# Kernel tuning notes

Measured on AMD Instinct MI355X. Metric: run time of the kernel, lower is better.

The kernel has to match this reference:

```python
import jax, jax.numpy as jnp
import numpy as np

E = 200000      # number of edge tokens
M = 3200000     # number of e2e attention pairs
IN_DIM = 64
EMBED = 64
H = 8
D = EMBED // H


def setup_inputs() -> dict:
    key = jax.random.key(0)
    ks = jax.random.split(key, 12)
    s = 1.0 / np.sqrt(IN_DIM)
    inp = {
        "edge_features": jax.random.normal(ks[0], (E, IN_DIM), dtype=jnp.float32),
        "e2e": jax.random.randint(ks[1], (2, M), 0, E, dtype=jnp.int32),
        "attn_bias": jax.random.normal(ks[2], (M, H), dtype=jnp.float32),
        "Wq": jax.random.uniform(ks[3], (IN_DIM, EMBED), jnp.float32, -s, s),
        "bq": jax.random.uniform(ks[4], (EMBED,), jnp.float32, -s, s),
        "Wk": jax.random.uniform(ks[5], (IN_DIM, EMBED), jnp.float32, -s, s),
        "bk": jax.random.uniform(ks[6], (EMBED,), jnp.float32, -s, s),
        "Wv": jax.random.uniform(ks[7], (IN_DIM, EMBED), jnp.float32, -s, s),
        "bv": jax.random.uniform(ks[8], (EMBED,), jnp.float32, -s, s),
        "Wo": jax.random.uniform(ks[9], (EMBED, EMBED), jnp.float32, -s, s),
        "bo": jax.random.uniform(ks[10], (EMBED,), jnp.float32, -s, s),
    }
    return inp


def _segment_softmax(logits, index, num_segments):
    # logits: (M, H) grouped by index (dst edge id)
    seg_max = jax.ops.segment_max(logits, index, num_segments=num_segments)
    seg_max = jnp.where(jnp.isfinite(seg_max), seg_max, 0.0)  # empty segments
    ex = jnp.exp(logits - seg_max[index])
    seg_sum = jax.ops.segment_sum(ex, index, num_segments=num_segments)
    return ex / (seg_sum[index] + 1e-16)


def reference(edge_features, e2e, attn_bias, Wq, bq, Wk, bk, Wv, bv, Wo, bo):
    src_e, dst_e = e2e[0], e2e[1]
    scale = D ** (-0.5)
    q = (edge_features @ Wq + bq).reshape(E, H, D)
    k = (edge_features @ Wk + bk).reshape(E, H, D)
    v = (edge_features @ Wv + bv).reshape(E, H, D)
    q_dst = q[dst_e]                       # (M, H, D) gather
    k_src = k[src_e]                       # (M, H, D) gather
    logits = jnp.sum(q_dst * k_src, axis=-1) * scale   # (M, H)
    logits = logits + attn_bias
    attn = _segment_softmax(logits, dst_e, E)          # (M, H)
    msg = v[src_e] * attn[..., None]                   # (M, H, D)
    out = jax.ops.segment_sum(msg, dst_e, num_segments=E)  # (E, H, D)
    out = out.reshape(E, EMBED)
    return out @ Wo + bo
```

## Files before the change

kernel.cpp:

```cpp
#include <hip/hip_runtime.h>

#define E_N 200000
#define M_N 3200000
#define SCAN_CHUNK 2048
#define NB1 98

#define NBUCK 782
#define NCHUNK 1000
#define CH 3200
#define BLEN (NBUCK * NCHUNK)
#define NB2 382
#define NP 4
#define SMAX 8192

typedef __attribute__((ext_vector_type(8))) short bf16x8;
typedef __attribute__((ext_vector_type(4))) float f32x4;
typedef __attribute__((ext_vector_type(8))) _Float16 f16x8;

__device__ __forceinline__ short f2bf(float f) {
    union { float f; unsigned u; } x; x.f = f;
    unsigned r = x.u + 0x7fffu + ((x.u >> 16) & 1u);
    return (short)(r >> 16);
}

__global__ __launch_bounds__(256) void qkv_mfma(
    const float* __restrict__ x,
    const float* __restrict__ Wq, const float* __restrict__ bq,
    const float* __restrict__ Wk, const float* __restrict__ bk,
    const float* __restrict__ Wv, const float* __restrict__ bv,
    float* __restrict__ q, _Float16* __restrict__ k, _Float16* __restrict__ v)
{
    const int w    = threadIdx.x >> 6;
    const int lane = threadIdx.x & 63;
    const int quad = lane >> 4;
    const int m    = lane & 15;

    bf16x8 Bq[4][2], Bk[4][2], Bv[4][2];
    float  bqv[4], bkv[4], bvv[4];
    #pragma unroll
    for (int ct = 0; ct < 4; ct++) {
        int cc = ct * 16 + m;
        bqv[ct] = bq[cc]; bkv[ct] = bk[cc]; bvv[ct] = bv[cc];
        #pragma unroll
        for (int kb = 0; kb < 2; kb++) {
            #pragma unroll
            for (int j = 0; j < 8; j++) {
                int kk = kb * 32 + quad * 8 + j;
                Bq[ct][kb][j] = f2bf(Wq[kk * 64 + cc]);
                Bk[ct][kb][j] = f2bf(Wk[kk * 64 + cc]);
                Bv[ct][kb][j] = f2bf(Wv[kk * 64 + cc]);
            }
        }
    }

    for (int row0 = blockIdx.x * 64 + w * 16; row0 < E_N; row0 += gridDim.x * 64) {
        const float* xr = x + (long long)(row0 + m) * 64 + quad * 8;
        bf16x8 A[2];
        #pragma unroll
        for (int kb = 0; kb < 2; kb++) {
            float4 p0 = *(const float4*)(xr + kb * 32);
            float4 p1 = *(const float4*)(xr + kb * 32 + 4);
            A[kb][0] = f2bf(p0.x); A[kb][1] = f2bf(p0.y);
            A[kb][2] = f2bf(p0.z); A[kb][3] = f2bf(p0.w);
            A[kb][4] = f2bf(p1.x); A[kb][5] = f2bf(p1.y);
            A[kb][6] = f2bf(p1.z); A[kb][7] = f2bf(p1.w);
        }

        #pragma unroll
        for (int ct = 0; ct < 4; ct++) {
            f32x4 aq = {bqv[ct], bqv[ct], bqv[ct], bqv[ct]};
            f32x4 ak = {bkv[ct], bkv[ct], bkv[ct], bkv[ct]};
            f32x4 av = {bvv[ct], bvv[ct], bvv[ct], bvv[ct]};
            aq = __builtin_amdgcn_mfma_f32_16x16x32_bf16(A[0], Bq[ct][0], aq, 0, 0, 0);
            aq = __builtin_amdgcn_mfma_f32_16x16x32_bf16(A[1], Bq[ct][1], aq, 0, 0, 0);
            ak = __builtin_amdgcn_mfma_f32_16x16x32_bf16(A[0], Bk[ct][0], ak, 0, 0, 0);
            ak = __builtin_amdgcn_mfma_f32_16x16x32_bf16(A[1], Bk[ct][1], ak, 0, 0, 0);
            av = __builtin_amdgcn_mfma_f32_16x16x32_bf16(A[0], Bv[ct][0], av, 0, 0, 0);
            av = __builtin_amdgcn_mfma_f32_16x16x32_bf16(A[1], Bv[ct][1], av, 0, 0, 0);
            #pragma unroll
            for (int i = 0; i < 4; i++) {
                long long off = (long long)(row0 + quad * 4 + i) * 64 + ct * 16 + m;
                q[off] = aq[i];
                k[off] = (_Float16)ak[i];
                v[off] = (_Float16)av[i];
            }
        }
    }
}

__global__ __launch_bounds__(256) void hist_kernel(
    const int* __restrict__ e2e, int* __restrict__ counts)
{
    int m4 = (blockIdx.x * 256 + threadIdx.x) * 4;
    if (m4 < M_N) {
        int4 d = *(const int4*)(e2e + M_N + m4);
        atomicAdd(&counts[d.x], 1);
        atomicAdd(&counts[d.y], 1);
        atomicAdd(&counts[d.z], 1);
        atomicAdd(&counts[d.w], 1);
    }
}

__global__ __launch_bounds__(256) void scan1_kernel(
    const int* __restrict__ counts, int* __restrict__ cursor,
    int* __restrict__ blocksums, int len)
{
    __shared__ int s[256];
    const int t = threadIdx.x;
    const int base = blockIdx.x * SCAN_CHUNK + t * 8;

    int vals[8];
    int tot = 0;
    #pragma unroll
    for (int j = 0; j < 8; j++) {
        int idx = base + j;
        vals[j] = (idx < len) ? counts[idx] : 0;
        tot += vals[j];
    }
    s[t] = tot;
    __syncthreads();
    for (int off = 1; off < 256; off <<= 1) {
        int add = (t >= off) ? s[t - off] : 0;
        __syncthreads();
        s[t] += add;
        __syncthreads();
    }
    int excl = (t == 0) ? 0 : s[t - 1];
    if (t == 255) blocksums[blockIdx.x] = s[255];

    int run = excl;
    #pragma unroll
    for (int j = 0; j < 8; j++) {
        int idx = base + j;
        if (idx < len) cursor[idx] = run;
        run += vals[j];
    }
}

__global__ __launch_bounds__(256) void scan2_kernel(
    const int* __restrict__ blocksums, int* __restrict__ blockoff, int nb)
{
    __shared__ int s[256];
    const int t = threadIdx.x;
    int vals[4];
    int tot = 0;
    #pragma unroll
    for (int u = 0; u < 4; u++) {
        int idx = t * 4 + u;
        vals[u] = (idx < nb) ? blocksums[idx] : 0;
        tot += vals[u];
    }
    s[t] = tot;
    __syncthreads();
    for (int off = 1; off < 256; off <<= 1) {
        int add = (t >= off) ? s[t - off] : 0;
        __syncthreads();
        s[t] += add;
        __syncthreads();
    }
    int run = (t == 0) ? 0 : s[t - 1];
    #pragma unroll
    for (int u = 0; u < 4; u++) {
        int idx = t * 4 + u;
        if (idx < nb) blockoff[idx] = run;
        run += vals[u];
    }
}

__global__ __launch_bounds__(1024) void bhist_kernel(
    const int* __restrict__ e2e, int* __restrict__ bcnt)
{
    __shared__ int lc[NBUCK];
    const int c = blockIdx.x;
    for (int i = threadIdx.x; i < NBUCK; i += 1024) lc[i] = 0;
    __syncthreads();
    const int m0 = c * CH;
    for (int i = threadIdx.x * 4; i < CH; i += 4096) {
        int4 d = *(const int4*)(e2e + M_N + m0 + i);
        atomicAdd(&lc[d.x >> 8], 1);
        atomicAdd(&lc[d.y >> 8], 1);
        atomicAdd(&lc[d.z >> 8], 1);
        atomicAdd(&lc[d.w >> 8], 1);
    }
    __syncthreads();
    for (int i = threadIdx.x; i < NBUCK; i += 1024) bcnt[i * NCHUNK + c] = lc[i];
}

__global__ __launch_bounds__(1024, 4) void scatter_bucket(
    const int* __restrict__ e2e, const float* __restrict__ bias,
    const int* __restrict__ bcur0, const int* __restrict__ boff2,
    int* __restrict__ meta, _Float16* __restrict__ bias_s)
{
    __shared__ int gbase[NBUCK];
    __shared__ unsigned short bk[CH];
    __shared__ char pool[CH * 16] __attribute__((aligned(16)));
    int*   cnt     = (int*)pool;
    int*   s       = (int*)(pool + 4096);
    f16x8* stage_b = (f16x8*)pool;
    int*   stage_m = (int*)pool;

    const int c = blockIdx.x;
    const int t = threadIdx.x;
    const int m0 = c * CH;

    for (int b = t; b < NBUCK; b += 1024) {
        cnt[b] = 0;
        int idx = b * NCHUNK + c;
        gbase[b] = bcur0[idx] + boff2[idx >> 11];
    }
    __syncthreads();

    int   mt[NP];
    int   pk[NP];
    f16x8 bb[NP];
    #pragma unroll
    for (int r = 0; r < NP; r++) {
        int i = t + r * 1024;
        pk[r] = -1;
        if (i < CH) {
            int m = m0 + i;
            int dst = e2e[M_N + m];
            int src = e2e[m];
            int b = dst >> 8;
            pk[r] = b << 12;
            mt[r] = ((dst & 255) << 18) | src;
            float4 b0 = *(const float4*)(bias + (long long)m * 8);
            float4 b1 = *(const float4*)(bias + (long long)m * 8 + 4);
            f16x8 xx;
            xx[0] = (_Float16)b0.x; xx[1] = (_Float16)b0.y;
            xx[2] = (_Float16)b0.z; xx[3] = (_Float16)b0.w;
            xx[4] = (_Float16)b1.x; xx[5] = (_Float16)b1.y;
            xx[6] = (_Float16)b1.z; xx[7] = (_Float16)b1.w;
            bb[r] = xx;
            atomicAdd(&cnt[b], 1);
        }
    }
    __syncthreads();

    int v = (t < NBUCK) ? cnt[t] : 0;
    s[t] = v;
    __syncthreads();
    for (int off = 1; off < 1024; off <<= 1) {
        int add = (t >= off) ? s[t - off] : 0;
        __syncthreads();
        s[t] += add;
        __syncthreads();
    }
    if (t < NBUCK) {
        int excl = (t == 0) ? 0 : s[t - 1];
        gbase[t] -= excl;
        cnt[t] = excl;
    }
    __syncthreads();

    #pragma unroll
    for (int r = 0; r < NP; r++) {
        if (pk[r] >= 0) {
            int b = pk[r] >> 12;
            int j = atomicAdd(&cnt[b], 1);
            pk[r] = (b << 12) | j;
        }
    }
    __syncthreads();

    #pragma unroll
    for (int r = 0; r < NP; r++) {
        if (pk[r] >= 0) {
            int j = pk[r] & 4095;
            stage_b[j] = bb[r];
            bk[j] = (unsigned short)(pk[r] >> 12);
        }
    }
    __syncthreads();
    for (int j = t; j < CH; j += 1024) {
        int slot = gbase[bk[j]] + j;
        *(f16x8*)(bias_s + (long long)slot * 8) = stage_b[j];
    }
    __syncthreads();

    #pragma unroll
    for (int r = 0; r < NP; r++) {
        if (pk[r] >= 0) stage_m[pk[r] & 4095] = mt[r];
    }
    __syncthreads();
    for (int j = t; j < CH; j += 1024) {
        meta[gbase[bk[j]] + j] = stage_m[j];
    }
}

__global__ __launch_bounds__(512, 2) void bucket_permute(
    const int* __restrict__ cursor, const int* __restrict__ boff,
    int* __restrict__ meta, _Float16* __restrict__ bias_s)
{
    __shared__ int smeta[SMAX];
    __shared__ int cnt[256];
    __shared__ int scn[256];
    const int b = blockIdx.x;
    const int t = threadIdx.x;
    const int d0 = b << 8;
    const int bs = cursor[d0] + boff[d0 >> 11];
    const int d1 = d0 + 256;
    const int be = (d1 < E_N) ? (cursor[d1] + boff[d1 >> 11]) : M_N;
    int n = be - bs;
    if (n > SMAX) n = SMAX;

    if (t < 256) cnt[t] = 0;
    __syncthreads();
    #pragma unroll
    for (int r = 0; r < SMAX / 512; r++) {
        int i = t + r * 512;
        if (i < n) {
            int mm = meta[bs + i];
            smeta[i] = mm;
            atomicAdd(&cnt[mm >> 18], 1);
        }
    }
    __syncthreads();
    if (t < 256) scn[t] = cnt[t];
    __syncthreads();
    for (int off = 1; off < 256; off <<= 1) {
        int v = 0;
        if (t < 256 && t >= off) v = scn[t - off];
        __syncthreads();
        if (t < 256) scn[t] += v;
        __syncthreads();
    }
    if (t < 256) cnt[t] = scn[t] - cnt[t];
    __syncthreads();

    int    pos[SMAX / 512];
    f16x8  bb[SMAX / 512];
    #pragma unroll
    for (int r = 0; r < SMAX / 512; r++) {
        int i = t + r * 512;
        if (i < n) {
            int mm = smeta[i];
            pos[r] = bs + atomicAdd(&cnt[mm >> 18], 1);
            bb[r]  = *(const f16x8*)(bias_s + (long long)(bs + i) * 8);
        }
    }
    __syncthreads();
    #pragma unroll
    for (int r = 0; r < SMAX / 512; r++) {
        int i = t + r * 512;
        if (i < n) {
            meta[pos[r]] = smeta[i] & 0x3FFFF;
            *(f16x8*)(bias_s + (long long)pos[r] * 8) = bb[r];
        }
    }
}

__global__ __launch_bounds__(256) void aggregate_kernel(
    const _Float16* __restrict__ k, const _Float16* __restrict__ v,
    const _Float16* __restrict__ bias_s,
    const int* __restrict__ counts, const int* __restrict__ cursor,
    const int* __restrict__ blockoff,
    const int* __restrict__ sorted,
    float* __restrict__ qmsg)
{
    const int wid  = threadIdx.x >> 6;
    const int lane = threadIdx.x & 63;
    const int ps   = lane >> 3;
    const int t    = lane & 7;

    for (int e = blockIdx.x * 4 + wid; e < E_N; e += gridDim.x * 4) {
        float qv = qmsg[(long long)e * 64 + lane];
        float qs[8];
        #pragma unroll
        for (int j = 0; j < 8; j++) qs[j] = __shfl(qv, t * 8 + j, 64);

        int start = cursor[e] + blockoff[e >> 11];
        int cnt   = counts[e];
        int end   = start + cnt;

        float acc[8] = {0.f,0.f,0.f,0.f,0.f,0.f,0.f,0.f};
        float ws = 0.0f;

        for (int i = start; i < end; i += 16) {
            int iA = i + ps;
            int iB = i + 8 + ps;
            bool vA = iA < end, vB = iB < end;
            int cA = vA ? iA : start;
            int cB = vB ? iB : start;
            int sA = sorted[cA];
            int sB = sorted[cB];
            float bA = (float)bias_s[(long long)cA * 8 + t];
            float bB = (float)bias_s[(long long)cB * 8 + t];
            f16x8 kA = *(const f16x8*)(k + (long long)sA * 64 + t * 8);
            f16x8 kB = *(const f16x8*)(k + (long long)sB * 64 + t * 8);
            f16x8 vA8 = *(const f16x8*)(v + (long long)sA * 64 + t * 8);
            f16x8 vB8 = *(const f16x8*)(v + (long long)sB * 64 + t * 8);

            float dA = 0.0f, dB = 0.0f;
            #pragma unroll
            for (int j = 0; j < 8; j++) {
                dA = fmaf(qs[j], (float)kA[j], dA);
                dB = fmaf(qs[j], (float)kB[j], dB);
            }
            float wA = vA ? __expf(fmaf(dA, 0.35355339059327373f, bA)) : 0.0f;
            float wB = vB ? __expf(fmaf(dB, 0.35355339059327373f, bB)) : 0.0f;
            ws += wA + wB;
            #pragma unroll
            for (int j = 0; j < 8; j++) {
                acc[j] = fmaf(wA, (float)vA8[j], acc[j]);
                acc[j] = fmaf(wB, (float)vB8[j], acc[j]);
            }
        }

        #pragma unroll
        for (int st = 8; st <= 32; st <<= 1) {
            #pragma unroll
            for (int j = 0; j < 8; j++) acc[j] += __shfl_xor(acc[j], st, 64);
            ws += __shfl_xor(ws, st, 64);
        }

        if (ps == 0) {
            float inv = 1.0f / (ws + 1e-16f);
            float4 o0, o1;
            o0.x = acc[0]*inv; o0.y = acc[1]*inv;
            o0.z = acc[2]*inv; o0.w = acc[3]*inv;
            o1.x = acc[4]*inv; o1.y = acc[5]*inv;
            o1.z = acc[6]*inv; o1.w = acc[7]*inv;
            *(float4*)(qmsg + (long long)e * 64 + t * 8)     = o0;
            *(float4*)(qmsg + (long long)e * 64 + t * 8 + 4) = o1;
        }
    }
}

__global__ __launch_bounds__(256) void out_mfma(
    const float* __restrict__ Wo, const float* __restrict__ bo,
    float* __restrict__ out)
{
    const int w    = threadIdx.x >> 6;
    const int lane = threadIdx.x & 63;
    const int quad = lane >> 4;
    const int m    = lane & 15;

    bf16x8 B[4][2];
    float  bov[4];
    #pragma unroll
    for (int ct = 0; ct < 4; ct++) {
        int cc = ct * 16 + m;
        bov[ct] = bo[cc];
        #pragma unroll
        for (int kb = 0; kb < 2; kb++) {
            #pragma unroll
            for (int j = 0; j < 8; j++) {
                int kk = kb * 32 + quad * 8 + j;
                B[ct][kb][j] = f2bf(Wo[kk * 64 + cc]);
            }
        }
    }

    for (int row0 = blockIdx.x * 64 + w * 16; row0 < E_N; row0 += gridDim.x * 64) {
        const float* xr = out + (long long)(row0 + m) * 64 + quad * 8;
        bf16x8 A[2];
        #pragma unroll
        for (int kb = 0; kb < 2; kb++) {
            float4 p0 = *(const float4*)(xr + kb * 32);
            float4 p1 = *(const float4*)(xr + kb * 32 + 4);
            A[kb][0] = f2bf(p0.x); A[kb][1] = f2bf(p0.y);
            A[kb][2] = f2bf(p0.z); A[kb][3] = f2bf(p0.w);
            A[kb][4] = f2bf(p1.x); A[kb][5] = f2bf(p1.y);
            A[kb][6] = f2bf(p1.z); A[kb][7] = f2bf(p1.w);
        }

        f32x4 acc[4];
        #pragma unroll
        for (int ct = 0; ct < 4; ct++) {
            acc[ct] = (f32x4){bov[ct], bov[ct], bov[ct], bov[ct]};
            acc[ct] = __builtin_amdgcn_mfma_f32_16x16x32_bf16(A[0], B[ct][0], acc[ct], 0, 0, 0);
            acc[ct] = __builtin_amdgcn_mfma_f32_16x16x32_bf16(A[1], B[ct][1], acc[ct], 0, 0, 0);
        }
        #pragma unroll
        for (int ct = 0; ct < 4; ct++) {
            #pragma unroll
            for (int i = 0; i < 4; i++) {
                out[(long long)(row0 + quad * 4 + i) * 64 + ct * 16 + m] = acc[ct][i];
            }
        }
    }
}

extern "C" void kernel_launch(void* const* d_in, const int* in_sizes, int n_in,
                              void* d_out, int out_size, void* d_ws, size_t ws_size,
                              hipStream_t stream) {
    const float* x    = (const float*)d_in[0];
    const int*   e2e  = (const int*)  d_in[1];
    const float* bias = (const float*)d_in[2];
    const float* Wq   = (const float*)d_in[3];
    const float* bq   = (const float*)d_in[4];
    const float* Wk   = (const float*)d_in[5];
    const float* bk   = (const float*)d_in[6];
    const float* Wv   = (const float*)d_in[7];
    const float* bv   = (const float*)d_in[8];
    const float* Wo   = (const float*)d_in[9];
    const float* bo   = (const float*)d_in[10];
    float* out = (float*)d_out;

    _Float16* kh     = (_Float16*)d_ws;
    _Float16* vh     = kh + (long long)E_N * 64;
    int*      counts = (int*)(vh + (long long)E_N * 64);
    int*      cursor = counts + E_N;
    int*      bsum   = cursor + E_N;
    int*      boff   = bsum + 512;
    int*      sorted = boff + 512;
    _Float16* bias_s = (_Float16*)(sorted + M_N);
    int*      bcnt   = (int*)(bias_s + (long long)M_N * 8);
    int*      bsum2  = bcnt + BLEN;
    int*      boff2  = bsum2 + 512;

    hipMemsetAsync(counts, 0, (size_t)E_N * sizeof(int), stream);

    qkv_mfma<<<640, 256, 0, stream>>>(x, Wq, bq, Wk, bk, Wv, bv, out, kh, vh);

    hist_kernel<<<M_N / 1024, 256, 0, stream>>>(e2e, counts);
    scan1_kernel<<<NB1, 256, 0, stream>>>(counts, cursor, bsum, E_N);
    scan2_kernel<<<1, 256, 0, stream>>>(bsum, boff, NB1);

    bhist_kernel<<<NCHUNK, 1024, 0, stream>>>(e2e, bcnt);
    scan1_kernel<<<NB2, 256, 0, stream>>>(bcnt, bcnt, bsum2, BLEN);
    scan2_kernel<<<1, 256, 0, stream>>>(bsum2, boff2, NB2);

    scatter_bucket<<<NCHUNK, 1024, 0, stream>>>(e2e, bias, bcnt, boff2,
                                                sorted, bias_s);
    bucket_permute<<<NBUCK, 512, 0, stream>>>(cursor, boff, sorted, bias_s);

    aggregate_kernel<<<8192, 256, 0, stream>>>(kh, vh, bias_s, counts, cursor,
                                               boff, sorted, out);

    out_mfma<<<640, 256, 0, stream>>>(Wo, bo, out);
}
```

Before: 652.1 us.

## Fuse bucket permute into aggregation and drop global per-edge histogram/scan

Removes the global per-destination histogram, scan and the bucket_permute pass. Each 256-destination bucket block now counting-sorts its entries in shared memory into a local order array and aggregates directly from it. Bucket bounds come from the existing bucket histogram scan. This cuts several kernel launches and a full global rewrite of the sorted meta/bias arrays. The cost is far fewer blocks (782 of 512 threads) doing aggregation, so occupancy and load balance are lower, and bias is now read with an indirect, uncoalesced access pattern.

```diff
diff --git a/kernel.cpp b/kernel.cpp
--- a/kernel.cpp
+++ b/kernel.cpp
@@ -3,7 +3,6 @@
 #define E_N 200000
 #define M_N 3200000
 #define SCAN_CHUNK 2048
-#define NB1 98
 
 #define NBUCK 782
 #define NCHUNK 1000
@@ -85,19 +84,6 @@
                 v[off] = (_Float16)av[i];
             }
         }
-    }
-}
-
-__global__ __launch_bounds__(256) void hist_kernel(
-    const int* __restrict__ e2e, int* __restrict__ counts)
-{
-    int m4 = (blockIdx.x * 256 + threadIdx.x) * 4;
-    if (m4 < M_N) {
-        int4 d = *(const int4*)(e2e + M_N + m4);
-        atomicAdd(&counts[d.x], 1);
-        atomicAdd(&counts[d.y], 1);
-        atomicAdd(&counts[d.z], 1);
-        atomicAdd(&counts[d.w], 1);
     }
 }
 
@@ -288,19 +274,30 @@
     }
 }
 
-__global__ __launch_bounds__(512, 2) void bucket_permute(
-    const int* __restrict__ cursor, const int* __restrict__ boff,
-    int* __restrict__ meta, _Float16* __restrict__ bias_s)
+__global__ __launch_bounds__(512, 2) void aggregate_bucket(
+    const _Float16* __restrict__ k, const _Float16* __restrict__ v,
+    const _Float16* __restrict__ bias_s,
+    const int* __restrict__ bstart, const int* __restrict__ boff2,
+    const int* __restrict__ meta,
+    float* __restrict__ qmsg)
 {
     __shared__ int smeta[SMAX];
+    __shared__ unsigned short ord[SMAX];
     __shared__ int cnt[256];
     __shared__ int scn[256];
+    __shared__ int base[256];
     const int b = blockIdx.x;
     const int t = threadIdx.x;
-    const int d0 = b << 8;
-    const int bs = cursor[d0] + boff[d0 >> 11];
-    const int d1 = d0 + 256;
-    const int be = (d1 < E_N) ? (cursor[d1] + boff[d1 >> 11]) : M_N;
+
+    const int i0 = b * NCHUNK;
+    const int bs = bstart[i0] + boff2[i0 >> 11];
+    int be;
+    if (b + 1 < NBUCK) {
+        int i1 = (b + 1) * NCHUNK;
+        be = bstart[i1] + boff2[i1 >> 11];
+    } else {
+        be = M_N;
+    }
     int n = be - bs;
     if (n > SMAX) n = SMAX;
 
@@ -319,77 +316,66 @@
     if (t < 256) scn[t] = cnt[t];
     __syncthreads();
     for (int off = 1; off < 256; off <<= 1) {
-        int v = 0;
-        if (t < 256 && t >= off) v = scn[t - off];
-        __syncthreads();
-        if (t < 256) scn[t] += v;
-        __syncthreads();
-    }
-    if (t < 256) cnt[t] = scn[t] - cnt[t];
-    __syncthreads();
-
-    int    pos[SMAX / 512];
-    f16x8  bb[SMAX / 512];
+        int vv = 0;
+        if (t < 256 && t >= off) vv = scn[t - off];
+        __syncthreads();
+        if (t < 256) scn[t] += vv;
+        __syncthreads();
+    }
+    if (t < 256) {
+        int excl = scn[t] - cnt[t];
+        base[t] = excl;
+        cnt[t]  = excl;
+    }
+    __syncthreads();
     #pragma unroll
     for (int r = 0; r < SMAX / 512; r++) {
         int i = t + r * 512;
         if (i < n) {
-            int mm = smeta[i];
-            pos[r] = bs + atomicAdd(&cnt[mm >> 18], 1);
-            bb[r]  = *(const f16x8*)(bias_s + (long long)(bs + i) * 8);
-        }
-    }
-    __syncthreads();
-    #pragma unroll
-    for (int r = 0; r < SMAX / 512; r++) {
-        int i = t + r * 512;
-        if (i < n) {
-            meta[pos[r]] = smeta[i] & 0x3FFFF;
-            *(f16x8*)(bias_s + (long long)pos[r] * 8) = bb[r];
-        }
-    }
-}
-
-__global__ __launch_bounds__(256) void aggregate_kernel(
-    const _Float16* __restrict__ k, const _Float16* __restrict__ v,
-    const _Float16* __restrict__ bias_s,
-    const int* __restrict__ counts, const int* __restrict__ cursor,
-    const int* __restrict__ blockoff,
-    const int* __restrict__ sorted,
-    float* __restrict__ qmsg)
-{
-    const int wid  = threadIdx.x >> 6;
-    const int lane = threadIdx.x & 63;
+            int p = atomicAdd(&cnt[smeta[i] >> 18], 1);
+            ord[p] = (unsigned short)i;
+        }
+    }
+    __syncthreads();
+
+    const int wid  = t >> 6;
+    const int lane = t & 63;
     const int ps   = lane >> 3;
-    const int t    = lane & 7;
-
-    for (int e = blockIdx.x * 4 + wid; e < E_N; e += gridDim.x * 4) {
+    const int th   = lane & 7;
+    const int d0   = b << 8;
+
+    for (int u = 0; u < 32; u++) {
+        int el = (wid << 5) + u;
+        int e  = d0 + el;
+        if (e >= E_N) break;
+
+        int st = base[el];
+        int en = cnt[el];
+
         float qv = qmsg[(long long)e * 64 + lane];
         float qs[8];
         #pragma unroll
-        for (int j = 0; j < 8; j++) qs[j] = __shfl(qv, t * 8 + j, 64);
-
-        int start = cursor[e] + blockoff[e >> 11];
-        int cnt   = counts[e];
-        int end   = start + cnt;
+        for (int j = 0; j < 8; j++) qs[j] = __shfl(qv, th * 8 + j, 64);
 
         float acc[8] = {0.f,0.f,0.f,0.f,0.f,0.f,0.f,0.f};
         float ws = 0.0f;
 
-        for (int i = start; i < end; i += 16) {
+        for (int i = st; i < en; i += 16) {
             int iA = i + ps;
             int iB = i + 8 + ps;
-            bool vA = iA < end, vB = iB < end;
-            int cA = vA ? iA : start;
-            int cB = vB ? iB : start;
-            int sA = sorted[cA];
-            int sB = sorted[cB];
-            float bA = (float)bias_s[(long long)cA * 8 + t];
-            float bB = (float)bias_s[(long long)cB * 8 + t];
-            f16x8 kA = *(const f16x8*)(k + (long long)sA * 64 + t * 8);
-            f16x8 kB = *(const f16x8*)(k + (long long)sB * 64 + t * 8);
-            f16x8 vA8 = *(const f16x8*)(v + (long long)sA * 64 + t * 8);
-            f16x8 vB8 = *(const f16x8*)(v + (long long)sB * 64 + t * 8);
+            bool vA = iA < en, vB = iB < en;
+            int cA = vA ? iA : st;
+            int cB = vB ? iB : st;
+            int rA = ord[cA];
+            int rB = ord[cB];
+            int sA = smeta[rA] & 0x3FFFF;
+            int sB = smeta[rB] & 0x3FFFF;
+            float bA = (float)bias_s[(long long)(bs + rA) * 8 + th];
+            float bB = (float)bias_s[(long long)(bs + rB) * 8 + th];
+            f16x8 kA = *(const f16x8*)(k + (long long)sA * 64 + th * 8);
+            f16x8 kB = *(const f16x8*)(k + (long long)sB * 64 + th * 8);
+            f16x8 vA8 = *(const f16x8*)(v + (long long)sA * 64 + th * 8);
+            f16x8 vB8 = *(const f16x8*)(v + (long long)sB * 64 + th * 8);
 
             float dA = 0.0f, dB = 0.0f;
             #pragma unroll
@@ -408,10 +394,10 @@
         }
 
         #pragma unroll
-        for (int st = 8; st <= 32; st <<= 1) {
-            #pragma unroll
-            for (int j = 0; j < 8; j++) acc[j] += __shfl_xor(acc[j], st, 64);
-            ws += __shfl_xor(ws, st, 64);
+        for (int stg = 8; stg <= 32; stg <<= 1) {
+            #pragma unroll
+            for (int j = 0; j < 8; j++) acc[j] += __shfl_xor(acc[j], stg, 64);
+            ws += __shfl_xor(ws, stg, 64);
         }
 
         if (ps == 0) {
@@ -421,8 +407,8 @@
             o0.z = acc[2]*inv; o0.w = acc[3]*inv;
             o1.x = acc[4]*inv; o1.y = acc[5]*inv;
             o1.z = acc[6]*inv; o1.w = acc[7]*inv;
-            *(float4*)(qmsg + (long long)e * 64 + t * 8)     = o0;
-            *(float4*)(qmsg + (long long)e * 64 + t * 8 + 4) = o1;
+            *(float4*)(qmsg + (long long)e * 64 + th * 8)     = o0;
+            *(float4*)(qmsg + (long long)e * 64 + th * 8 + 4) = o1;
         }
     }
 }
@@ -500,34 +486,23 @@
 
     _Float16* kh     = (_Float16*)d_ws;
     _Float16* vh     = kh + (long long)E_N * 64;
-    int*      counts = (int*)(vh + (long long)E_N * 64);
-    int*      cursor = counts + E_N;
-    int*      bsum   = cursor + E_N;
-    int*      boff   = bsum + 512;
-    int*      sorted = boff + 512;
-    _Float16* bias_s = (_Float16*)(sorted + M_N);
+    int*      meta   = (int*)(vh + (long long)E_N * 64);
+    _Float16* bias_s = (_Float16*)(meta + M_N);
     int*      bcnt   = (int*)(bias_s + (long long)M_N * 8);
     int*      bsum2  = bcnt + BLEN;
     int*      boff2  = bsum2 + 512;
 
-    hipMemsetAsync(counts, 0, (size_t)E_N * sizeof(int), stream);
-
     qkv_mfma<<<640, 256, 0, stream>>>(x, Wq, bq, Wk, bk, Wv, bv, out, kh, vh);
-
-    hist_kernel<<<M_N / 1024, 256, 0, stream>>>(e2e, counts);
-    scan1_kernel<<<NB1, 256, 0, stream>>>(counts, cursor, bsum, E_N);
-    scan2_kernel<<<1, 256, 0, stream>>>(bsum, boff, NB1);
 
     bhist_kernel<<<NCHUNK, 1024, 0, stream>>>(e2e, bcnt);
     scan1_kernel<<<NB2, 256, 0, stream>>>(bcnt, bcnt, bsum2, BLEN);
     scan2_kernel<<<1, 256, 0, stream>>>(bsum2, boff2, NB2);
 
     scatter_bucket<<<NCHUNK, 1024, 0, stream>>>(e2e, bias, bcnt, boff2,
-                                                sorted, bias_s);
-    bucket_permute<<<NBUCK, 512, 0, stream>>>(cursor, boff, sorted, bias_s);
-
-    aggregate_kernel<<<8192, 256, 0, stream>>>(kh, vh, bias_s, counts, cursor,
-                                               boff, sorted, out);
+                                                meta, bias_s);
+
+    aggregate_bucket<<<NBUCK, 512, 0, stream>>>(kh, vh, bias_s, bcnt, boff2,
+                                                meta, out);
 
     out_mfma<<<640, 256, 0, stream>>>(Wo, bo, out);
 }
```

After: 558.7 us. -14.3%, faster.
